# Kernel tuning notes

Measured on AMD Instinct MI355X. Metric: run time of the kernel, lower is better.

## Reference

```python
import jax, jax.numpy as jnp
import numpy as np

N_NODES = 100000
N_EDGES = 1600000
IN_CH = 128
OUT_CH = 128
N_REL = 8


def setup_inputs() -> dict:
    key = jax.random.key(0)
    k1, k2, k3, k4, k5, k6 = jax.random.split(key, 6)
    x = jax.random.normal(k1, (N_NODES, IN_CH), dtype=jnp.float32)
    edge_index = jax.random.randint(k2, (2, N_EDGES), 0, N_NODES, dtype=jnp.int64)
    edge_type = jax.random.randint(k3, (N_EDGES,), 0, N_REL, dtype=jnp.int64)
    # learned parameters (PyG RGCNConv: per-relation weight, root weight, bias)
    scale = 1.0 / np.sqrt(IN_CH)
    weight = jax.random.normal(k4, (N_REL, IN_CH, OUT_CH), dtype=jnp.float32) * scale
    root = jax.random.normal(k5, (IN_CH, OUT_CH), dtype=jnp.float32) * scale
    bias = jax.random.normal(k6, (OUT_CH,), dtype=jnp.float32) * 0.01
    return {"x": x, "edge_index": edge_index, "edge_type": edge_type,
            "weight": weight, "root": root, "bias": bias}


def reference(x, edge_index, edge_type, weight, root, bias):
    # PyG RGCNConv forward: out_i = x_i @ root + bias
    #   + sum_r mean_{j in N_r(i)} (x_j @ W_r)   (default aggr='mean' per relation)
    N = x.shape[0]
    R, _, O = weight.shape
    src, dst = edge_index[0], edge_index[1]
    # transform all nodes under every relation once: [R, N, O]
    xW = jnp.einsum('ni,rio->rno', x, weight)
    msg = xW[edge_type, src]                      # [E, O] per-edge message
    seg = edge_type * N + dst                     # segment per (relation, dst)
    sums = jax.ops.segment_sum(msg, seg, num_segments=R * N)        # [R*N, O]
    cnt = jax.ops.segment_sum(jnp.ones_like(msg[:, 0]), seg, num_segments=R * N)
    mean = sums / jnp.maximum(cnt, 1.0)[:, None]
    agg = mean.reshape(R, N, O).sum(axis=0)       # sum over relations
    return agg + x @ root + bias
```

## Files before the change

kernel.cpp:

```cpp
#include <hip/hip_runtime.h>
#include <hip/hip_bf16.h>
#include <stdint.h>

#define N_NODES 100000
#define N_EDGES 1600000
#define CH 128
#define N_REL 8
#define N_PAD 100096
#define N_KEYS (N_NODES * N_REL)

#define NBKT 782
#define NCHUNK 782
#define CHUNK_E 2048
#define CELL_CAP 20
#define NSLOT (NBKT * CELL_CAP)
#define SENT 0xFFFFFFFFu
#define PERM_LDS_CAP 4096

using frag_ab = __attribute__((ext_vector_type(8))) short;
using frag_cd = __attribute__((ext_vector_type(4))) float;

__device__ __forceinline__ short f2bs(float f) {
    union { __hip_bfloat16 h; short s; } u;
    u.h = __float2bfloat16(f);
    return u.s;
}

__device__ __forceinline__ uint32_t pack2bf(float a, float b) {
    union { __hip_bfloat16 h; unsigned short s; } ua, ub;
    ua.h = __float2bfloat16(a); ub.h = __float2bfloat16(b);
    return (uint32_t)ua.s | ((uint32_t)ub.s << 16);
}

__device__ __forceinline__ float bf_lo(uint32_t u) { return __uint_as_float(u << 16); }
__device__ __forceinline__ float bf_hi(uint32_t u) { return __uint_as_float(u & 0xffff0000u); }


__global__ __launch_bounds__(256)
void prep_kernel(const int* __restrict__ ei, const int* __restrict__ et,
                 uint32_t* __restrict__ ents,
                 const float* __restrict__ x, short* __restrict__ xb,
                 const float* __restrict__ root, const float* __restrict__ W,
                 short* __restrict__ Bsw) {
    __shared__ uint32_t cell[NSLOT];
    __shared__ int cur[NBKT];
    const int tid = threadIdx.x;
    const int c = blockIdx.x;
    const int g = blockIdx.x * 256 + tid;

    if (c < NCHUNK) {
        for (int i = tid; i < NSLOT; i += 256) cell[i] = SENT;
        for (int i = tid; i < NBKT; i += 256) cur[i] = 0;
        __syncthreads();
#pragma unroll
        for (int j = 0; j < 8; ++j) {
            const int e = c * CHUNK_E + j * 256 + tid;
            if (e < N_EDGES) {
                const int dst = ei[N_EDGES + e];
                const int src = ei[e];
                const int r = et[e];
                const int b = dst >> 7;
                const int pos = atomicAdd(&cur[b], 1);
                if (pos < CELL_CAP)
                    cell[b * CELL_CAP + pos] =
                        ((uint32_t)src << 10) | ((uint32_t)(dst & 127) << 3) | (uint32_t)r;
            }
        }
        __syncthreads();
        uint32_t* dst_g = ents + (size_t)c * NSLOT;
        for (int i = tid; i < NSLOT; i += 256) dst_g[i] = cell[i];
    }

    if (g < N_NODES * CH / 8) {
        const float4* xp = (const float4*)x;
        float4 a = xp[(size_t)g * 2], bb = xp[(size_t)g * 2 + 1];
        frag_ab f;
        f[0] = f2bs(a.x); f[1] = f2bs(a.y); f[2] = f2bs(a.z); f[3] = f2bs(a.w);
        f[4] = f2bs(bb.x); f[5] = f2bs(bb.y); f[6] = f2bs(bb.z); f[7] = f2bs(bb.w);
        *(frag_ab*)(xb + (size_t)g * 8) = f;
    }

    if (g < 9 * 2048) {
        int chunk = g >> 11, entry = g & 2047;
        int m16 = entry & 15, ct = (entry >> 4) & 7, quad = (entry >> 7) & 3, ks = entry >> 9;
        const float* src = (chunk == 0) ? root : W + (size_t)(chunk - 1) * CH * CH;
        int col = ct * 16 + m16, kb = ks * 32 + quad * 8;
        frag_ab f;
#pragma unroll
        for (int j = 0; j < 8; ++j) f[j] = f2bs(src[(size_t)(kb + j) * CH + col]);
        *(frag_ab*)(Bsw + (size_t)g * 8) = f;
    }
}


__global__ __launch_bounds__(512)
void bin_kernel(const uint32_t* __restrict__ ents,
                int* __restrict__ perm_g, int* __restrict__ ends_g) {
    __shared__ uint32_t stage[PERM_LDS_CAP];
    __shared__ int hist[1024];
    __shared__ int cursor[1024];
    __shared__ int shl[512];
    __shared__ int ncomp;
    const int tid = threadIdx.x;
    const int lane = tid & 63;
    const int b = blockIdx.x;

    hist[tid] = 0; hist[tid + 512] = 0;
    if (tid == 0) ncomp = 0;
    __syncthreads();
    for (int j = tid; j < NCHUNK * CELL_CAP; j += 512) {
        const int c = j / CELL_CAP, i = j - c * CELL_CAP;
        const uint32_t v = ents[(size_t)c * NSLOT + b * CELL_CAP + i];
        const bool hit = (v != SENT);
        const unsigned long long m = __ballot(hit);
        if (m) {
            const int leader = __ffsll((long long)m) - 1;
            int base = 0;
            if (lane == leader) base = atomicAdd(&ncomp, __popcll(m));
            base = __shfl(base, leader);
            if (hit) {
                const int pos = base + __popcll(m & ((1ULL << lane) - 1ULL));
                if (pos < PERM_LDS_CAP) stage[pos] = v;
            }
        }
    }
    __syncthreads();
    int n = ncomp; if (n > PERM_LDS_CAP) n = PERM_LDS_CAP;
    for (int i = tid; i < n; i += 512) atomicAdd(&hist[stage[i] & 1023], 1);
    __syncthreads();
    const int h0 = hist[2 * tid], h1 = hist[2 * tid + 1];
    const int s2 = h0 + h1;
    shl[tid] = s2;
    __syncthreads();
    for (int st = 1; st < 512; st <<= 1) {
        int u = (tid >= st) ? shl[tid - st] : 0;
        __syncthreads();
        shl[tid] += u;
        __syncthreads();
    }
    const int excl = shl[tid] - s2;
    cursor[2 * tid]     = excl;
    cursor[2 * tid + 1] = excl + h0;
    {
        int e1 = excl + h0, e2 = excl + h0 + h1;
        ends_g[(size_t)b * 1024 + 2 * tid]     = (e1 > PERM_LDS_CAP) ? PERM_LDS_CAP : e1;
        ends_g[(size_t)b * 1024 + 2 * tid + 1] = (e2 > PERM_LDS_CAP) ? PERM_LDS_CAP : e2;
    }
    __syncthreads();
    for (int i = tid; i < n; i += 512) {
        const uint32_t v = stage[i];
        const int pos = atomicAdd(&cursor[v & 1023], 1);
        if (pos < PERM_LDS_CAP) perm_g[(size_t)b * PERM_LDS_CAP + pos] = (int)(v >> 10);
    }
}

#define ACC_U4(U, B)                                            \
    do {                                                        \
        a[(B)+0] += bf_lo((U).x); a[(B)+1] += bf_hi((U).x);     \
        a[(B)+2] += bf_lo((U).y); a[(B)+3] += bf_hi((U).y);     \
        a[(B)+4] += bf_lo((U).z); a[(B)+5] += bf_hi((U).z);     \
        a[(B)+6] += bf_lo((U).w); a[(B)+7] += bf_hi((U).w);     \
    } while (0)

__global__ __launch_bounds__(512, 4)
void rgcn_fused(const int* __restrict__ ends_g, const int* __restrict__ perm_g,
                const short* __restrict__ xb, const short* __restrict__ Bsw,
                const float* __restrict__ bias, float* __restrict__ out) {
    __shared__ short Ash[128 * 128];
    __shared__ int perm_lds[PERM_LDS_CAP];
    __shared__ int lends[1025];
    const int tid = threadIdx.x;
    const int wave = tid >> 6, lane = tid & 63;
    const int m16 = lane & 15, quad = lane >> 4;
    const int wm = wave >> 2, wn = wave & 3;
    const int b = blockIdx.x;
    const long B0 = (long)b * 128;

    if (tid == 0) { lends[0] = 0; perm_lds[0] = 0; }
    for (int i = tid; i < 1024; i += 512) lends[1 + i] = ends_g[(size_t)b * 1024 + i];
    __syncthreads();
    const int nperm = lends[1024];
    for (int i = tid; i < nperm; i += 512) perm_lds[i] = perm_g[(size_t)b * PERM_LDS_CAP + i];

    float bcol[2];
#pragma unroll
    for (int ct = 0; ct < 2; ++ct) bcol[ct] = bias[wn * 32 + ct * 16 + m16];

    frag_cd acc[4][2];
#pragma unroll
    for (int mt = 0; mt < 4; ++mt)
#pragma unroll
        for (int ct = 0; ct < 2; ++ct) acc[mt][ct] = (frag_cd){0.f, 0.f, 0.f, 0.f};

#pragma unroll
    for (int ks = 0; ks < 4; ++ks) {
        frag_ab af[4];
#pragma unroll
        for (int mt = 0; mt < 4; ++mt)
            af[mt] = *(const frag_ab*)(xb + (B0 + wm * 64 + mt * 16 + m16) * CH + ks * 32 + quad * 8);
#pragma unroll
        for (int ct = 0; ct < 2; ++ct) {
            frag_ab bf = *(const frag_ab*)(Bsw + (size_t)((((ks * 4 + quad) * 8) + wn * 2 + ct) * 16 + m16) * 8);
#pragma unroll
            for (int mt = 0; mt < 4; ++mt)
                acc[mt][ct] = __builtin_amdgcn_mfma_f32_16x16x32_bf16(af[mt], bf, acc[mt][ct], 0, 0, 0);
        }
    }
    __syncthreads();

    const int lrow = tid >> 2;
    const int q4 = tid & 3;
    const uint32_t ch64 = (uint32_t)q4 << 6;
    const char* xbp = (const char*)xb;
    char* drow = (char*)Ash + lrow * 256;
    const int swz = lrow & 7;

    for (int r = 0; r < N_REL; ++r) {
        const int keyL = lrow * 8 + r;
        const int s = lends[keyL];
        const int e = lends[keyL + 1];
        float a[32];
#pragma unroll
        for (int i = 0; i < 32; ++i) a[i] = 0.f;
        int p0 = perm_lds[(s < e) ? s : 0];
        int p1 = perm_lds[(s + 1 < e) ? s + 1 : ((s < e) ? s : 0)];
        for (int k = s; k < e; k += 2) {
            const char* c0 = xbp + (((size_t)(uint32_t)p0 << 8) | ch64);
            const char* c1 = xbp + (((size_t)(uint32_t)p1 << 8) | ch64);
            const uint4 u0 = *(const uint4*)(c0);
            const uint4 u1 = *(const uint4*)(c0 + 16);
            const uint4 u2 = *(const uint4*)(c0 + 32);
            const uint4 u3 = *(const uint4*)(c0 + 48);
            const uint4 u4 = *(const uint4*)(c1);
            const uint4 u5 = *(const uint4*)(c1 + 16);
            const uint4 u6 = *(const uint4*)(c1 + 32);
            const uint4 u7 = *(const uint4*)(c1 + 48);
            const bool two = (k + 1 < e);
            const int kn = k + 2;
            p0 = perm_lds[(kn < e) ? kn : 0];
            p1 = perm_lds[(kn + 1 < e) ? kn + 1 : 0];
            ACC_U4(u0, 0); ACC_U4(u1, 8); ACC_U4(u2, 16); ACC_U4(u3, 24);
            if (two) { ACC_U4(u4, 0); ACC_U4(u5, 8); ACC_U4(u6, 16); ACC_U4(u7, 24); }
        }
        const int c = e - s;
        const float sc = (c > 1) ? (1.0f / (float)c) : 1.0f;
#pragma unroll
        for (int t = 0; t < 4; ++t) {
            uint4 w;
            w.x = pack2bf(a[t * 8 + 0] * sc, a[t * 8 + 1] * sc);
            w.y = pack2bf(a[t * 8 + 2] * sc, a[t * 8 + 3] * sc);
            w.z = pack2bf(a[t * 8 + 4] * sc, a[t * 8 + 5] * sc);
            w.w = pack2bf(a[t * 8 + 6] * sc, a[t * 8 + 7] * sc);
            *(uint4*)(drow + (((q4 * 4 + t) ^ swz) << 4)) = w;
        }
        __syncthreads();
        const short* Bc = Bsw + (size_t)(r + 1) * 2048 * 8;
#pragma unroll
        for (int ks = 0; ks < 4; ++ks) {
            frag_ab af[4];
#pragma unroll
            for (int mt = 0; mt < 4; ++mt) {
                const int lr = wm * 64 + mt * 16 + m16;
                af[mt] = *(const frag_ab*)((const char*)Ash + lr * 256 + (((ks * 4 + quad) ^ (lr & 7)) << 4));
            }
#pragma unroll
            for (int ct = 0; ct < 2; ++ct) {
                frag_ab bf = *(const frag_ab*)(Bc + (size_t)((((ks * 4 + quad) * 8) + wn * 2 + ct) * 16 + m16) * 8);
#pragma unroll
                for (int mt = 0; mt < 4; ++mt)
                    acc[mt][ct] = __builtin_amdgcn_mfma_f32_16x16x32_bf16(af[mt], bf, acc[mt][ct], 0, 0, 0);
            }
        }
        __syncthreads();
    }

#pragma unroll
    for (int mt = 0; mt < 4; ++mt) {
#pragma unroll
        for (int ct = 0; ct < 2; ++ct) {
            const long row0 = B0 + wm * 64 + mt * 16 + quad * 4;
            const int col = wn * 32 + ct * 16 + m16;
#pragma unroll
            for (int rg = 0; rg < 4; ++rg) {
                const long rr = row0 + rg;
                if (rr < N_NODES) out[rr * CH + col] = acc[mt][ct][rg] + bcol[ct];
            }
        }
    }
}


__global__ void count_rd_kernel(const int* __restrict__ ei, const int* __restrict__ et,
                                int* __restrict__ cnt) {
    int e = blockIdx.x * 256 + threadIdx.x;
    if (e < N_EDGES) {
        int dst = ei[N_EDGES + e];
        int r = et[e];
        atomicAdd(&cnt[r * N_NODES + dst], 1);
    }
}

__global__ void scatter_kernel(const int* __restrict__ ei, const int* __restrict__ et,
                               const float* __restrict__ x, float* __restrict__ sums,
                               int rel) {
    int gid = (blockIdx.x * 256 + threadIdx.x) >> 5;
    int lane = threadIdx.x & 31;
    int ngroups = gridDim.x * 8;
    for (int e = gid; e < N_EDGES; e += ngroups) {
        if (et[e] != rel) continue;
        int src = ei[e];
        int dst = ei[N_EDGES + e];
        float4 v = ((const float4*)(x + (size_t)src * CH))[lane];
        float* s = sums + (size_t)dst * CH + (size_t)lane * 4;
        atomicAdd(s + 0, v.x);
        atomicAdd(s + 1, v.y);
        atomicAdd(s + 2, v.z);
        atomicAdd(s + 3, v.w);
    }
}

__global__ __launch_bounds__(256, 2)
void gemm_kernel(const float* __restrict__ A, const float* __restrict__ B,
                 const float* __restrict__ bias, const int* __restrict__ cnt,
                 float* __restrict__ out, int accumulate) {
    const int wave = threadIdx.x >> 6;
    const int lane = threadIdx.x & 63;
    const int m16 = lane & 15;
    const int quad = lane >> 4;

    frag_ab bfrag[4][8];
#pragma unroll
    for (int ks = 0; ks < 4; ++ks) {
        const int kb = ks * 32 + quad * 8;
#pragma unroll
        for (int ct = 0; ct < 8; ++ct) {
            const int col = ct * 16 + m16;
            frag_ab f;
#pragma unroll
            for (int j = 0; j < 8; ++j)
                f[j] = f2bs(B[(size_t)(kb + j) * CH + col]);
            bfrag[ks][ct] = f;
        }
    }

    const int nstrips = (N_NODES + 63) / 64;
    for (int strip = blockIdx.x; strip < nstrips; strip += gridDim.x) {
        const int row = strip * 64 + wave * 16 + m16;
        const bool valid = row < N_NODES;
        float scale = 1.0f;
        if (cnt != nullptr && valid) {
            int c = cnt[row];
            if (c > 1) scale = 1.0f / (float)c;
        }
        const float4* arow = (const float4*)(A + (size_t)(valid ? row : 0) * CH);
        frag_cd acc[8];
#pragma unroll
        for (int ct = 0; ct < 8; ++ct) acc[ct] = (frag_cd){0.f, 0.f, 0.f, 0.f};
#pragma unroll
        for (int ks = 0; ks < 4; ++ks) {
            float4 a0 = arow[ks * 8 + quad * 2];
            float4 a1 = arow[ks * 8 + quad * 2 + 1];
            frag_ab af;
            af[0] = f2bs(a0.x * scale); af[1] = f2bs(a0.y * scale);
            af[2] = f2bs(a0.z * scale); af[3] = f2bs(a0.w * scale);
            af[4] = f2bs(a1.x * scale); af[5] = f2bs(a1.y * scale);
            af[6] = f2bs(a1.z * scale); af[7] = f2bs(a1.w * scale);
#pragma unroll
            for (int ct = 0; ct < 8; ++ct)
                acc[ct] = __builtin_amdgcn_mfma_f32_16x16x32_bf16(af, bfrag[ks][ct], acc[ct], 0, 0, 0);
        }
        const int obase = strip * 64 + wave * 16 + quad * 4;
#pragma unroll
        for (int ct = 0; ct < 8; ++ct) {
            const int col = ct * 16 + m16;
#pragma unroll
            for (int rg = 0; rg < 4; ++rg) {
                const int r = obase + rg;
                if (r < N_NODES) {
                    const size_t idx = (size_t)r * CH + col;
                    if (accumulate) out[idx] += acc[ct][rg];
                    else out[idx] = acc[ct][rg] + bias[col];
                }
            }
        }
    }
}

__global__ void edge_transform_kernel(const int* __restrict__ ei, const int* __restrict__ et,
                                      const float* __restrict__ x, const float* __restrict__ W,
                                      const int* __restrict__ cnt, float* __restrict__ out) {
    __shared__ float xs[CH];
    const int tid = threadIdx.x;
    for (int e = blockIdx.x; e < N_EDGES; e += gridDim.x) {
        const int src = ei[e];
        const int dst = ei[N_EDGES + e];
        const int r = et[e];
        __syncthreads();
        xs[tid] = x[(size_t)src * CH + tid];
        __syncthreads();
        const int c = cnt[r * N_NODES + dst];
        const float scale = (c > 1) ? (1.0f / (float)c) : 1.0f;
        const float* Wr = W + (size_t)r * CH * CH;
        float acc = 0.f;
#pragma unroll 8
        for (int k = 0; k < CH; ++k) acc += xs[k] * Wr[(size_t)k * CH + tid];
        atomicAdd(&out[(size_t)dst * CH + tid], acc * scale);
    }
}


static inline size_t al512(size_t x) { return (x + 511) & ~(size_t)511; }

extern "C" void kernel_launch(void* const* d_in, const int* in_sizes, int n_in,
                              void* d_out, int out_size, void* d_ws, size_t ws_size,
                              hipStream_t stream) {
    const float* x    = (const float*)d_in[0];
    const int*   ei   = (const int*)d_in[1];
    const int*   et   = (const int*)d_in[2];
    const float* W    = (const float*)d_in[3];
    const float* root = (const float*)d_in[4];
    const float* bias = (const float*)d_in[5];
    float* out = (float*)d_out;

    size_t o = 0;
    const size_t o_ents = o; o += al512((size_t)NCHUNK * NSLOT * 4);
    const size_t o_perm = o; o += al512((size_t)NBKT * PERM_LDS_CAP * 4);
    const size_t o_ends = o; o += al512((size_t)NBKT * 1024 * 4);
    const size_t o_bsw  = o; o += al512((size_t)9 * 2048 * 16);
    const size_t o_xb   = o; o += al512((size_t)N_PAD * CH * 2);
    const size_t need_t1 = o;

    const size_t cnt_bytes = (size_t)N_REL * N_NODES * sizeof(int);
    const size_t cnt_rsv   = al512(cnt_bytes);
    const size_t sums51    = (size_t)N_NODES * CH * sizeof(float);

    char* ws = (char*)d_ws;
    if (ws_size >= need_t1) {
        uint32_t* ents   = (uint32_t*)(ws + o_ents);
        int*      perm_g = (int*)(ws + o_perm);
        int*      ends_g = (int*)(ws + o_ends);
        short*    Bsw    = (short*)(ws + o_bsw);
        short*    xb     = (short*)(ws + o_xb);

        prep_kernel<<<(N_NODES * CH / 8 + 255) / 256, 256, 0, stream>>>(
            ei, et, ents, x, xb, root, W, Bsw);
        bin_kernel<<<NBKT, 512, 0, stream>>>(ents, perm_g, ends_g);
        rgcn_fused<<<NBKT, 512, 0, stream>>>(ends_g, perm_g, xb, Bsw, bias, out);
    } else if (ws_size >= cnt_rsv + sums51) {
        int*   cnt  = (int*)d_ws;
        float* sums = (float*)((char*)d_ws + cnt_rsv);
        hipMemsetAsync(cnt, 0, cnt_bytes, stream);
        count_rd_kernel<<<(N_EDGES + 255) / 256, 256, 0, stream>>>(ei, et, cnt);
        gemm_kernel<<<512, 256, 0, stream>>>(x, root, bias, nullptr, out, 0);
        for (int r = 0; r < N_REL; ++r) {
            hipMemsetAsync(sums, 0, sums51, stream);
            scatter_kernel<<<6400, 256, 0, stream>>>(ei, et, x, sums, r);
            gemm_kernel<<<512, 256, 0, stream>>>(sums, W + (size_t)r * CH * CH,
                                                 nullptr, cnt + (size_t)r * N_NODES, out, 1);
        }
    } else {
        int* cnt = (int*)d_ws;
        hipMemsetAsync(cnt, 0, cnt_bytes, stream);
        count_rd_kernel<<<(N_EDGES + 255) / 256, 256, 0, stream>>>(ei, et, cnt);
        gemm_kernel<<<512, 256, 0, stream>>>(x, root, bias, nullptr, out, 0);
        edge_transform_kernel<<<65536, CH, 0, stream>>>(ei, et, x, W, cnt, out);
    }
}
```

Before: 287.1 us.

## Replace sentinel-filled cells with per-chunk lengths and move x conversion into bin kernel

The prep kernel no longer fills shared cells with sentinels. It now writes a per-(chunk,bucket) length array and copies cells out with uint4 stores. Its grid shrinks from the x-conversion size (6250 blocks) to NCHUNK blocks. The bin kernel reads only valid entries guided by those lengths, skipping sentinel loads, and also does the fp32-to-bf16 conversion of x with a grid-stride loop. This cuts wasted global reads and block launches, at the cost of an extra lens array and extra work in bin_kernel ahead of binning.

```diff
diff --git a/kernel.cpp b/kernel.cpp
--- a/kernel.cpp
+++ b/kernel.cpp
@@ -14,7 +14,6 @@
 #define CHUNK_E 2048
 #define CELL_CAP 20
 #define NSLOT (NBKT * CELL_CAP)
-#define SENT 0xFFFFFFFFu
 #define PERM_LDS_CAP 4096
 
 using frag_ab = __attribute__((ext_vector_type(8))) short;
@@ -38,8 +37,7 @@
 
 __global__ __launch_bounds__(256)
 void prep_kernel(const int* __restrict__ ei, const int* __restrict__ et,
-                 uint32_t* __restrict__ ents,
-                 const float* __restrict__ x, short* __restrict__ xb,
+                 uint32_t* __restrict__ ents, int* __restrict__ lens,
                  const float* __restrict__ root, const float* __restrict__ W,
                  short* __restrict__ Bsw) {
     __shared__ uint32_t cell[NSLOT];
@@ -48,38 +46,6 @@
     const int c = blockIdx.x;
     const int g = blockIdx.x * 256 + tid;
 
-    if (c < NCHUNK) {
-        for (int i = tid; i < NSLOT; i += 256) cell[i] = SENT;
-        for (int i = tid; i < NBKT; i += 256) cur[i] = 0;
-        __syncthreads();
-#pragma unroll
-        for (int j = 0; j < 8; ++j) {
-            const int e = c * CHUNK_E + j * 256 + tid;
-            if (e < N_EDGES) {
-                const int dst = ei[N_EDGES + e];
-                const int src = ei[e];
-                const int r = et[e];
-                const int b = dst >> 7;
-                const int pos = atomicAdd(&cur[b], 1);
-                if (pos < CELL_CAP)
-                    cell[b * CELL_CAP + pos] =
-                        ((uint32_t)src << 10) | ((uint32_t)(dst & 127) << 3) | (uint32_t)r;
-            }
-        }
-        __syncthreads();
-        uint32_t* dst_g = ents + (size_t)c * NSLOT;
-        for (int i = tid; i < NSLOT; i += 256) dst_g[i] = cell[i];
-    }
-
-    if (g < N_NODES * CH / 8) {
-        const float4* xp = (const float4*)x;
-        float4 a = xp[(size_t)g * 2], bb = xp[(size_t)g * 2 + 1];
-        frag_ab f;
-        f[0] = f2bs(a.x); f[1] = f2bs(a.y); f[2] = f2bs(a.z); f[3] = f2bs(a.w);
-        f[4] = f2bs(bb.x); f[5] = f2bs(bb.y); f[6] = f2bs(bb.z); f[7] = f2bs(bb.w);
-        *(frag_ab*)(xb + (size_t)g * 8) = f;
-    }
-
     if (g < 9 * 2048) {
         int chunk = g >> 11, entry = g & 2047;
         int m16 = entry & 15, ct = (entry >> 4) & 7, quad = (entry >> 7) & 3, ks = entry >> 9;
@@ -90,28 +56,71 @@
         for (int j = 0; j < 8; ++j) f[j] = f2bs(src[(size_t)(kb + j) * CH + col]);
         *(frag_ab*)(Bsw + (size_t)g * 8) = f;
     }
+
+    for (int i = tid; i < NBKT; i += 256) cur[i] = 0;
+    __syncthreads();
+#pragma unroll
+    for (int j = 0; j < 8; ++j) {
+        const int e = c * CHUNK_E + j * 256 + tid;
+        if (e < N_EDGES) {
+            const int dst = ei[N_EDGES + e];
+            const int src = ei[e];
+            const int r = et[e];
+            const int b = dst >> 7;
+            const int pos = atomicAdd(&cur[b], 1);
+            if (pos < CELL_CAP)
+                cell[b * CELL_CAP + pos] =
+                    ((uint32_t)src << 10) | ((uint32_t)(dst & 127) << 3) | (uint32_t)r;
+        }
+    }
+    __syncthreads();
+    for (int i = tid; i < NBKT; i += 256) {
+        int n = cur[i];
+        lens[(size_t)c * NBKT + i] = (n > CELL_CAP) ? CELL_CAP : n;
+    }
+    {
+        const uint4* cs = (const uint4*)cell;
+        uint4* dg = (uint4*)(ents + (size_t)c * NSLOT);
+        for (int i = tid; i < NSLOT / 4; i += 256) dg[i] = cs[i];
+    }
 }
 
 
 __global__ __launch_bounds__(512)
-void bin_kernel(const uint32_t* __restrict__ ents,
-                int* __restrict__ perm_g, int* __restrict__ ends_g) {
+void bin_kernel(const uint32_t* __restrict__ ents, const int* __restrict__ lens,
+                int* __restrict__ perm_g, int* __restrict__ ends_g,
+                const float* __restrict__ x, short* __restrict__ xb) {
     __shared__ uint32_t stage[PERM_LDS_CAP];
     __shared__ int hist[1024];
     __shared__ int cursor[1024];
     __shared__ int shl[512];
+    __shared__ int lens_l[NCHUNK];
     __shared__ int ncomp;
     const int tid = threadIdx.x;
     const int lane = tid & 63;
     const int b = blockIdx.x;
 
+    {
+        const int nst = NBKT * 512;
+        const float4* xp = (const float4*)x;
+        for (int gi = b * 512 + tid; gi < N_NODES * CH / 8; gi += nst) {
+            float4 a = xp[(size_t)gi * 2], bb = xp[(size_t)gi * 2 + 1];
+            frag_ab f;
+            f[0] = f2bs(a.x); f[1] = f2bs(a.y); f[2] = f2bs(a.z); f[3] = f2bs(a.w);
+            f[4] = f2bs(bb.x); f[5] = f2bs(bb.y); f[6] = f2bs(bb.z); f[7] = f2bs(bb.w);
+            *(frag_ab*)(xb + (size_t)gi * 8) = f;
+        }
+    }
+
+    for (int i = tid; i < NCHUNK; i += 512) lens_l[i] = lens[(size_t)i * NBKT + b];
     hist[tid] = 0; hist[tid + 512] = 0;
     if (tid == 0) ncomp = 0;
     __syncthreads();
     for (int j = tid; j < NCHUNK * CELL_CAP; j += 512) {
         const int c = j / CELL_CAP, i = j - c * CELL_CAP;
-        const uint32_t v = ents[(size_t)c * NSLOT + b * CELL_CAP + i];
-        const bool hit = (v != SENT);
+        const bool hit = (i < lens_l[c]);
+        uint32_t v = 0;
+        if (hit) v = ents[(size_t)c * NSLOT + b * CELL_CAP + i];
         const unsigned long long m = __ballot(hit);
         if (m) {
             const int leader = __ffsll((long long)m) - 1;
@@ -424,6 +433,7 @@
 
     size_t o = 0;
     const size_t o_ents = o; o += al512((size_t)NCHUNK * NSLOT * 4);
+    const size_t o_lens = o; o += al512((size_t)NCHUNK * NBKT * 4);
     const size_t o_perm = o; o += al512((size_t)NBKT * PERM_LDS_CAP * 4);
     const size_t o_ends = o; o += al512((size_t)NBKT * 1024 * 4);
     const size_t o_bsw  = o; o += al512((size_t)9 * 2048 * 16);
@@ -437,14 +447,14 @@
     char* ws = (char*)d_ws;
     if (ws_size >= need_t1) {
         uint32_t* ents   = (uint32_t*)(ws + o_ents);
+        int*      lens   = (int*)(ws + o_lens);
         int*      perm_g = (int*)(ws + o_perm);
         int*      ends_g = (int*)(ws + o_ends);
         short*    Bsw    = (short*)(ws + o_bsw);
         short*    xb     = (short*)(ws + o_xb);
 
-        prep_kernel<<<(N_NODES * CH / 8 + 255) / 256, 256, 0, stream>>>(
-            ei, et, ents, x, xb, root, W, Bsw);
-        bin_kernel<<<NBKT, 512, 0, stream>>>(ents, perm_g, ends_g);
+        prep_kernel<<<NCHUNK, 256, 0, stream>>>(ei, et, ents, lens, root, W, Bsw);
+        bin_kernel<<<NBKT, 512, 0, stream>>>(ents, lens, perm_g, ends_g, x, xb);
         rgcn_fused<<<NBKT, 512, 0, stream>>>(ends_g, perm_g, xb, Bsw, bias, out);
     } else if (ws_size >= cnt_rsv + sums51) {
         int*   cnt  = (int*)d_ws;
```

New measurement: 299.2 us. 4.2% more time.
